# Kernel tuning notes

Measured on AMD Instinct MI355X. Metric: run time of the kernel, lower is better.

Reference implementation:

```python
import jax, jax.numpy as jnp
import numpy as np

SAMPLE_RATE = 256
WIN = 64          # round(256*250/1000)
HOP = 32          # round(256*125/1000)
HIDDEN = 512
PER_CHAN = 8
MAX_CH = 64
_EEG_BANDS = ((0.5, 4.0), (4.0, 8.0), (8.0, 13.0), (13.0, 30.0), (30.0, 100.0))

_FREQS = np.fft.rfftfreq(WIN, d=1.0 / SAMPLE_RATE)
_BAND_MASKS = [np.logical_and(_FREQS >= lo, _FREQS < hi) for (lo, hi) in _EEG_BANDS]


def _sinusoidal_1d(n, dim, dtype=jnp.float32):
    pos = jnp.arange(n, dtype=jnp.float32)[:, None]
    half = dim // 2
    div = jnp.exp(jnp.arange(half, dtype=jnp.float32) * (-np.log(10000.0) / half))
    ang = pos * div[None, :]
    pe = jnp.zeros((n, dim), dtype=jnp.float32)
    pe = pe.at[:, 0::2].set(jnp.sin(ang))
    pe = pe.at[:, 1::2].set(jnp.cos(ang))
    return pe.astype(dtype)


def setup_inputs() -> dict:
    key = jax.random.key(0)
    k = jax.random.split(key, 5)
    B, T, C = 8, 65536, 64
    return {
        "signal": jax.random.normal(k[0], (B, T, C), dtype=jnp.float32),
        "chan_w": 0.02 * jax.random.normal(k[1], (MAX_CH, 7, PER_CHAN), dtype=jnp.float32),
        "chan_b": 0.02 * jax.random.normal(k[2], (MAX_CH, PER_CHAN), dtype=jnp.float32),
        "mix_w": 0.02 * jax.random.normal(k[3], (HIDDEN, MAX_CH * PER_CHAN), dtype=jnp.float32),
        "marker": 0.02 * jax.random.normal(k[4], (HIDDEN,), dtype=jnp.float32),
    }


def reference(signal, chan_w, chan_b, mix_w, marker):
    B, T, C = signal.shape  # C == MAX_CH, no padding/mask branch
    Tw = (T - WIN) // HOP + 1
    idx = jnp.arange(Tw)[:, None] * HOP + jnp.arange(WIN)[None, :]
    x = jnp.transpose(signal[:, idx, :], (0, 1, 3, 2))
    # spectral features
    mag = jnp.abs(jnp.fft.rfft(x, axis=-1))
    band_feats = jnp.stack(
        [mag[..., m].mean(axis=-1) if m.any() else jnp.zeros(mag.shape[:-1], mag.dtype)
         for m in _BAND_MASKS],
        axis=-1,
    )  # (B, Tw, C, 5)
    mean = x.mean(axis=-1, keepdims=True)
    std = jnp.std(x, axis=-1, ddof=1, keepdims=True)  # torch std is unbiased
    feats = jnp.concatenate([band_feats, mean, std], axis=-1)  # (B, Tw, C, 7)
    # per-channel projection + bias
    emb = jnp.einsum("btcf,cfp->btcp", feats, chan_w) + chan_b[None, None]
    flat = emb.reshape(B, Tw, MAX_CH * PER_CHAN)
    z = flat @ mix_w.T  # (B, Tw, HIDDEN)
    z = z + _sinusoidal_1d(Tw, HIDDEN, z.dtype)[None]
    mk = jnp.broadcast_to(marker[None, None, :], (B, 1, HIDDEN))
    return jnp.concatenate([mk, z], axis=1)  # (B, 1+Tw, HIDDEN)
```

## Files before the change

kernel.cpp:

```cpp
#include <hip/hip_runtime.h>
#include <stdint.h>

#define TW_N 2047
#define BATCH 8
#define T_LEN 65536
#define NCH 64
#define HID 512
#define NWIN (BATCH * TW_N)

typedef unsigned short ushortT;

__device__ __forceinline__ ushortT f2b(float f) {
  union { float f; uint32_t i; } v; v.f = f;
  uint32_t r = v.i + 0x7fffu + ((v.i >> 16) & 1u);
  return (ushortT)(r >> 16);
}
__device__ __forceinline__ uint32_t pk2(float lo, float hi) {
  return (uint32_t)f2b(lo) | ((uint32_t)f2b(hi) << 16);
}

__device__ __forceinline__ void gload_lds16(const void* g, void* l) {
  __builtin_amdgcn_global_load_lds(
      (const __attribute__((address_space(1))) uint32_t*)g,
      (__attribute__((address_space(3))) uint32_t*)l, 16, 0, 0);
}

constexpr float CQ[17] = {
  1.0f, 0.9951847267f, 0.9807852804f, 0.9569403357f, 0.9238795325f,
  0.8819212643f, 0.8314696123f, 0.7730104534f, 0.7071067812f, 0.6343932842f,
  0.5555702330f, 0.4713967368f, 0.3826834324f, 0.2902846773f, 0.1950903220f,
  0.0980171403f, 0.0f };
constexpr float cos64(int m) {
  m &= 63;
  return (m <= 16) ? CQ[m] : (m < 32) ? -CQ[32 - m] : (m < 48) ? -CQ[m - 32] : CQ[64 - m];
}
constexpr float sin64(int m) { return cos64(m - 16); }
struct TwTab { float c[24][32]; float s[24][32]; };
constexpr TwTab make_tab() {
  TwTab t{};
  for (int i = 0; i < 24; ++i)
    for (int j = 0; j < 32; ++j) {
      int m = ((i + 1) * j) & 63;
      t.c[i][j] = cos64(m);
      t.s[i][j] = sin64(m);
    }
  return t;
}
constexpr TwTab TT = make_tab();

__device__ ushortT Bpack[HID * HID];

__global__ __launch_bounds__(256) void prep_kernel(
    const float* __restrict__ marker, const float* __restrict__ Bw,
    float* __restrict__ out)
{
  const int gid = blockIdx.x * 256 + threadIdx.x;
  if (blockIdx.x < 16) {
    out[(size_t)(gid >> 9) * (2048 * 512) + (gid & 511)] = marker[gid & 511];
  } else {
    const int i = (gid - 4096) * 8;
    const float4 f0 = *(const float4*)(Bw + i);
    const float4 f1 = *(const float4*)(Bw + i + 4);
    uint4 u;
    u.x = pk2(f0.x, f0.y); u.y = pk2(f0.z, f0.w);
    u.z = pk2(f1.x, f1.y); u.w = pk2(f1.z, f1.w);
    *(uint4*)(Bpack + i) = u;
  }
}

__global__ __launch_bounds__(256) void feat_embed_kernel(
    const float* __restrict__ sig, const float* __restrict__ chw,
    const float* __restrict__ chb, ushortT* __restrict__ flatB)
{
  const int tid = threadIdx.x;
  const int c = tid & 63;
  const int gw = blockIdx.x * 4 + (tid >> 6);
  const int b = gw >> 8;
  const int run = gw & 255;
  const int tw0 = run * 8;
  const int nw = (tw0 + 8 <= TW_N) ? 8 : (TW_N - tw0);
  const float* sg = sig + ((size_t)b * T_LEN + (size_t)tw0 * 32) * NCH + c;
  const float* wr = chw + c * 56;

  float A[32], Bh[32], O[32], R[32];
#pragma unroll
  for (int t = 0; t < 32; ++t) A[t] = sg[t * 64];
#pragma unroll
  for (int t = 0; t < 32; ++t) Bh[t] = sg[(t + 32) * 64];

#pragma unroll 1
  for (int l = 0; l < nw; ++l) {
    {
      int hrow = (tw0 + l + 2) * 32;
      hrow = hrow < (T_LEN - 32) ? hrow : (T_LEN - 32);
      const float* pn = sig + ((size_t)b * T_LEN + hrow) * NCH + c;
#pragma unroll
      for (int t = 0; t < 32; ++t) R[t] = pn[t * 64];
    }

    float sum = 0.f, sumsq = 0.f;
#pragma unroll
    for (int t = 0; t < 32; ++t) {
      O[t] = A[t] - Bh[t];
      A[t] = A[t] + Bh[t];
      sum += A[t];
      sumsq = fmaf(A[t], A[t], fmaf(O[t], O[t], sumsq));
    }

    float b1 = 0.f, b2 = 0.f, b3 = 0.f, b4 = 0.f;
#pragma unroll
    for (int i = 0; i < 24; ++i) {
      const int k = i + 1;
      float re = 0.f, im = 0.f;
#pragma unroll
      for (int t = 0; t < 32; ++t) {
        const float v = (k & 1) ? O[t] : A[t];
        re = fmaf(v, TT.c[i][t], re);
        im = fmaf(v, TT.s[i][t], im);
      }
      const float mag = __builtin_amdgcn_sqrtf(fmaf(re, re, im * im));
      if (k == 1) b1 += mag;
      else if (k < 4) b2 += mag;
      else if (k < 8) b3 += mag;
      else b4 += mag;
    }

    const float mean = sum * (1.f / 64.f);
    const float var = (sumsq * 0.5f - sum * sum * (1.f / 64.f)) * (1.f / 63.f);
    const float sd = __builtin_amdgcn_sqrtf(fmaxf(var, 0.f));

    const float f1 = b1, f2 = b2 * 0.5f, f3 = b3 * 0.25f, f4 = b4 * (1.f / 17.f);
    float emb[8];
#pragma unroll
    for (int p = 0; p < 8; ++p) emb[p] = chb[c * 8 + p];
#pragma unroll
    for (int p = 0; p < 8; ++p) {
      float e = emb[p];
      e = fmaf(f1, wr[8 + p], e);
      e = fmaf(f2, wr[16 + p], e);
      e = fmaf(f3, wr[24 + p], e);
      e = fmaf(f4, wr[32 + p], e);
      e = fmaf(mean, wr[40 + p], e);
      e = fmaf(sd, wr[48 + p], e);
      emb[p] = e;
    }

    uint32_t pka[4];
#pragma unroll
    for (int q = 0; q < 4; ++q) pka[q] = pk2(emb[2 * q], emb[2 * q + 1]);
    const int w = b * TW_N + tw0 + l;
    *(uint4*)(flatB + (size_t)w * HID + c * 8) = make_uint4(pka[0], pka[1], pka[2], pka[3]);

#pragma unroll
    for (int t = 0; t < 32; ++t) { A[t] = Bh[t]; Bh[t] = R[t]; }
  }
}

typedef __attribute__((ext_vector_type(8))) short short8;
typedef __attribute__((ext_vector_type(4))) float f32x4;

__global__ __launch_bounds__(256) void mix_gemm_kernel(
    const ushortT* __restrict__ A,
    float* __restrict__ out)
{
  __shared__ ushortT As[3][128 * 32];
  __shared__ ushortT Bs[3][128 * 32];

  const int tid = threadIdx.x;
  const int lane = tid & 63;
  const int wv = tid >> 6;
  const int wm = wv >> 1, wn = wv & 1;
  const int fr = lane & 15;
  const int fq = lane >> 4;

  const int n0 = blockIdx.x * 128;
  const int m0 = blockIdx.y * 128;

  const int srow = tid >> 2;
  const int sko = (tid & 3) * 8;

  f32x4 acc[4][4];
#pragma unroll
  for (int i = 0; i < 4; ++i)
#pragma unroll
    for (int j = 0; j < 4; ++j) acc[i][j] = (f32x4){0.f, 0.f, 0.f, 0.f};

  int am0 = m0 + srow;       am0 = am0 < NWIN ? am0 : NWIN - 1;
  int am1 = m0 + 64 + srow;  am1 = am1 < NWIN ? am1 : NWIN - 1;
  const ushortT* ga0 = A + (size_t)am0 * HID + sko;
  const ushortT* ga1 = A + (size_t)am1 * HID + sko;
  const ushortT* gb0 = Bpack + (size_t)(n0 + srow) * HID + sko;
  const ushortT* gb1 = Bpack + (size_t)(n0 + 64 + srow) * HID + sko;

#define STAGE(buf, kt) do {                                                    \
    const int ko_ = (kt) * 32;                                                 \
    gload_lds16(ga0 + ko_, (char*)&As[buf][0] + tid * 16);                     \
    gload_lds16(ga1 + ko_, (char*)&As[buf][0] + 4096 + tid * 16);              \
    gload_lds16(gb0 + ko_, (char*)&Bs[buf][0] + tid * 16);                     \
    gload_lds16(gb1 + ko_, (char*)&Bs[buf][0] + 4096 + tid * 16);              \
  } while (0)

  STAGE(0, 0);
  STAGE(1, 1);

  int c0 = 0, c1 = 1, c2 = 2;
  for (int kt = 0; kt < 16; ++kt) {
    if (kt < 14) {
      STAGE(c2, kt + 2);
      asm volatile("s_waitcnt vmcnt(8)\n\ts_barrier" ::: "memory");
    } else if (kt == 14) {
      asm volatile("s_waitcnt vmcnt(4)\n\ts_barrier" ::: "memory");
    } else {
      asm volatile("s_waitcnt vmcnt(0)\n\ts_barrier" ::: "memory");
    }

    short8 af[4], bf[4];
#pragma unroll
    for (int mt = 0; mt < 4; ++mt)
      af[mt] = *(const short8*)&As[c0][(wm * 64 + mt * 16 + fr) * 32 + fq * 8];
#pragma unroll
    for (int nt = 0; nt < 4; ++nt)
      bf[nt] = *(const short8*)&Bs[c0][(wn * 64 + nt * 16 + fr) * 32 + fq * 8];
#pragma unroll
    for (int mt = 0; mt < 4; ++mt)
#pragma unroll
      for (int nt = 0; nt < 4; ++nt)
        acc[mt][nt] = __builtin_amdgcn_mfma_f32_16x16x32_bf16(af[mt], bf[nt], acc[mt][nt], 0, 0, 0);

    asm volatile("s_barrier" ::: "memory");
    const int tmp = c0; c0 = c1; c1 = c2; c2 = tmp;
  }
#undef STAGE

#pragma unroll
  for (int nt = 0; nt < 4; ++nt) {
    const int ng = n0 + wn * 64 + nt * 16 + fr;
    const float dv = __expf(-0.03597789208f * (float)(ng >> 1));
    const bool odd = (ng & 1);
#pragma unroll
    for (int mt = 0; mt < 4; ++mt) {
#pragma unroll
      for (int r = 0; r < 4; ++r) {
        const int mg = m0 + wm * 64 + mt * 16 + fq * 4 + r;
        if (mg < NWIN) {
          const int bb = mg / TW_N;
          const int tw = mg - bb * TW_N;
          const float ang = (float)tw * dv;
          const float pev = odd ? __cosf(ang) : __sinf(ang);
          out[((size_t)(bb * 2048 + 1 + tw)) * HID + ng] = acc[mt][nt][r] + pev;
        }
      }
    }
  }
}

extern "C" void kernel_launch(void* const* d_in, const int* in_sizes, int n_in,
                              void* d_out, int out_size, void* d_ws, size_t ws_size,
                              hipStream_t stream)
{
  const float* sig = (const float*)d_in[0];
  const float* chw = (const float*)d_in[1];
  const float* chb = (const float*)d_in[2];
  const float* mxw = (const float*)d_in[3];
  const float* mkr = (const float*)d_in[4];
  float* out = (float*)d_out;

  ushortT* flatB = (ushortT*)d_ws;

  hipLaunchKernelGGL(prep_kernel, dim3(144), dim3(256), 0, stream, mkr, mxw, out);
  hipLaunchKernelGGL(feat_embed_kernel, dim3(512), dim3(256), 0, stream, sig, chw, chb, flatB);
  hipLaunchKernelGGL(mix_gemm_kernel, dim3(4, 128), dim3(256), 0, stream, flatB, out);
}
```

Measured before the change: 249.8 us.

## Add second radix-2 split to windowed DFT and double feature kernel parallelism

```diff
diff --git a/kernel.cpp b/kernel.cpp
--- a/kernel.cpp
+++ b/kernel.cpp
@@ -35,18 +35,22 @@
   return (m <= 16) ? CQ[m] : (m < 32) ? -CQ[32 - m] : (m < 48) ? -CQ[m - 32] : CQ[64 - m];
 }
 constexpr float sin64(int m) { return cos64(m - 16); }
-struct TwTab { float c[24][32]; float s[24][32]; };
-constexpr TwTab make_tab() {
-  TwTab t{};
-  for (int i = 0; i < 24; ++i)
-    for (int j = 0; j < 32; ++j) {
-      int m = ((i + 1) * j) & 63;
-      t.c[i][j] = cos64(m);
-      t.s[i][j] = sin64(m);
+struct Tw2 { float oc[12][32]; float os[12][32]; float ec[12][16]; float es[12][16]; };
+constexpr Tw2 make2() {
+  Tw2 t{};
+  for (int i = 0; i < 12; ++i)
+    for (int tt = 0; tt < 32; ++tt) {
+      t.oc[i][tt] = cos64((2 * i + 1) * tt);
+      t.os[i][tt] = sin64((2 * i + 1) * tt);
+    }
+  for (int j = 1; j <= 12; ++j)
+    for (int tt = 0; tt < 16; ++tt) {
+      t.ec[j - 1][tt] = cos64(2 * j * tt);
+      t.es[j - 1][tt] = sin64(2 * j * tt);
     }
   return t;
 }
-constexpr TwTab TT = make_tab();
+constexpr Tw2 TW = make2();
 
 __device__ ushortT Bpack[HID * HID];
 
@@ -68,91 +72,106 @@
   }
 }
 
-__global__ __launch_bounds__(256) void feat_embed_kernel(
+#define WIN_BODY(X, Y, l, pf_ofs) do {                                        \
+    float sum = 0.f, so2 = 0.f, se2 = 0.f;                                    \
+    _Pragma("unroll")                                                         \
+    for (int t = 0; t < 32; ++t) {                                            \
+      O[t] = X[t] - Y[t];                                                     \
+      X[t] = X[t] + Y[t];                                                     \
+      so2 = fmaf(O[t], O[t], so2);                                            \
+    }                                                                         \
+    _Pragma("unroll")                                                         \
+    for (int t = 0; t < 16; ++t) {                   \
+      const float u = X[t] + X[t + 16], v = X[t] - X[t + 16];                 \
+      X[t] = u; X[t + 16] = v;                                                \
+      sum += u;                                                               \
+      se2 = fmaf(u, u, fmaf(v, v, se2));                                      \
+    }                                                                         \
+    float b1 = 0.f, b2 = 0.f, b3 = 0.f, b4 = 0.f;                             \
+    _Pragma("unroll")                                                         \
+    for (int j = 1; j <= 12; ++j) {                          \
+      float re = 0.f, im = 0.f;                                               \
+      _Pragma("unroll")                                                       \
+      for (int t = 0; t < 16; ++t) {                                          \
+        const float v = X[(j & 1) * 16 + t];                 \
+        re = fmaf(v, TW.ec[j - 1][t], re);                                    \
+        im = fmaf(v, TW.es[j - 1][t], im);                                    \
+      }                                                                       \
+      const float mag = __builtin_amdgcn_sqrtf(fmaf(re, re, im * im));        \
+      const int k = 2 * j;                                                    \
+      if (k < 4) b2 += mag; else if (k < 8) b3 += mag; else b4 += mag;        \
+    }                                                                         \
+    if ((pf_ofs) >= 0) {                        \
+      const float* pn = sg + (size_t)(pf_ofs) * (32 * NCH);                   \
+      _Pragma("unroll")                                                       \
+      for (int t = 0; t < 32; ++t) X[t] = pn[t * 64];                         \
+    }                                                                         \
+    _Pragma("unroll")                                                         \
+    for (int i = 0; i < 12; ++i) {                  \
+      float re = 0.f, im = 0.f;                                               \
+      _Pragma("unroll")                                                       \
+      for (int t = 0; t < 32; ++t) {                                          \
+        re = fmaf(O[t], TW.oc[i][t], re);                                     \
+        im = fmaf(O[t], TW.os[i][t], im);                                     \
+      }                                                                       \
+      const float mag = __builtin_amdgcn_sqrtf(fmaf(re, re, im * im));        \
+      const int k = 2 * i + 1;                                                \
+      if (k == 1) b1 += mag;                                                  \
+      else if (k < 4) b2 += mag;                                              \
+      else if (k < 8) b3 += mag;                                              \
+      else b4 += mag;                                                         \
+    }                                                                         \
+    const float mean = sum * (1.f / 64.f);                                    \
+    const float var =                                                         \
+        (se2 * 0.25f + so2 * 0.5f - sum * sum * (1.f / 64.f)) * (1.f / 63.f); \
+    const float sd = __builtin_amdgcn_sqrtf(fmaxf(var, 0.f));                 \
+    const float f1 = b1, f2 = b2 * 0.5f, f3 = b3 * 0.25f,                     \
+                f4 = b4 * (1.f / 17.f);                                       \
+    float emb[8];                                                             \
+    _Pragma("unroll")                                                         \
+    for (int p = 0; p < 8; ++p) {                                             \
+      float e = cbp[p];                                                       \
+      e = fmaf(f1, wr[8 + p], e);                                             \
+      e = fmaf(f2, wr[16 + p], e);                                            \
+      e = fmaf(f3, wr[24 + p], e);                                            \
+      e = fmaf(f4, wr[32 + p], e);                                            \
+      e = fmaf(mean, wr[40 + p], e);                                          \
+      e = fmaf(sd, wr[48 + p], e);                                            \
+      emb[p] = e;                                                             \
+    }                                                                         \
+    uint32_t pka[4];                                                          \
+    _Pragma("unroll")                                                         \
+    for (int q = 0; q < 4; ++q) pka[q] = pk2(emb[2 * q], emb[2 * q + 1]);     \
+    *(uint4*)(flatB + (size_t)(wbase + (l)) * HID + c * 8) =                  \
+        make_uint4(pka[0], pka[1], pka[2], pka[3]);                           \
+  } while (0)
+
+__global__ __launch_bounds__(256, 4) void feat_embed_kernel(
     const float* __restrict__ sig, const float* __restrict__ chw,
     const float* __restrict__ chb, ushortT* __restrict__ flatB)
 {
   const int tid = threadIdx.x;
   const int c = tid & 63;
   const int gw = blockIdx.x * 4 + (tid >> 6);
-  const int b = gw >> 8;
-  const int run = gw & 255;
-  const int tw0 = run * 8;
-  const int nw = (tw0 + 8 <= TW_N) ? 8 : (TW_N - tw0);
+  const int b = gw >> 9;
+  const int r = gw & 511;
+  int tw0 = r * 4;
+  if (tw0 > TW_N - 4) tw0 = TW_N - 4;
+  const int wbase = b * TW_N + tw0;
   const float* sg = sig + ((size_t)b * T_LEN + (size_t)tw0 * 32) * NCH + c;
   const float* wr = chw + c * 56;
-
-  float A[32], Bh[32], O[32], R[32];
+  const float* cbp = chb + c * 8;
+
+  float A[32], Bh[32], O[32];
 #pragma unroll
   for (int t = 0; t < 32; ++t) A[t] = sg[t * 64];
 #pragma unroll
   for (int t = 0; t < 32; ++t) Bh[t] = sg[(t + 32) * 64];
 
 #pragma unroll 1
-  for (int l = 0; l < nw; ++l) {
-    {
-      int hrow = (tw0 + l + 2) * 32;
-      hrow = hrow < (T_LEN - 32) ? hrow : (T_LEN - 32);
-      const float* pn = sig + ((size_t)b * T_LEN + hrow) * NCH + c;
-#pragma unroll
-      for (int t = 0; t < 32; ++t) R[t] = pn[t * 64];
-    }
-
-    float sum = 0.f, sumsq = 0.f;
-#pragma unroll
-    for (int t = 0; t < 32; ++t) {
-      O[t] = A[t] - Bh[t];
-      A[t] = A[t] + Bh[t];
-      sum += A[t];
-      sumsq = fmaf(A[t], A[t], fmaf(O[t], O[t], sumsq));
-    }
-
-    float b1 = 0.f, b2 = 0.f, b3 = 0.f, b4 = 0.f;
-#pragma unroll
-    for (int i = 0; i < 24; ++i) {
-      const int k = i + 1;
-      float re = 0.f, im = 0.f;
-#pragma unroll
-      for (int t = 0; t < 32; ++t) {
-        const float v = (k & 1) ? O[t] : A[t];
-        re = fmaf(v, TT.c[i][t], re);
-        im = fmaf(v, TT.s[i][t], im);
-      }
-      const float mag = __builtin_amdgcn_sqrtf(fmaf(re, re, im * im));
-      if (k == 1) b1 += mag;
-      else if (k < 4) b2 += mag;
-      else if (k < 8) b3 += mag;
-      else b4 += mag;
-    }
-
-    const float mean = sum * (1.f / 64.f);
-    const float var = (sumsq * 0.5f - sum * sum * (1.f / 64.f)) * (1.f / 63.f);
-    const float sd = __builtin_amdgcn_sqrtf(fmaxf(var, 0.f));
-
-    const float f1 = b1, f2 = b2 * 0.5f, f3 = b3 * 0.25f, f4 = b4 * (1.f / 17.f);
-    float emb[8];
-#pragma unroll
-    for (int p = 0; p < 8; ++p) emb[p] = chb[c * 8 + p];
-#pragma unroll
-    for (int p = 0; p < 8; ++p) {
-      float e = emb[p];
-      e = fmaf(f1, wr[8 + p], e);
-      e = fmaf(f2, wr[16 + p], e);
-      e = fmaf(f3, wr[24 + p], e);
-      e = fmaf(f4, wr[32 + p], e);
-      e = fmaf(mean, wr[40 + p], e);
-      e = fmaf(sd, wr[48 + p], e);
-      emb[p] = e;
-    }
-
-    uint32_t pka[4];
-#pragma unroll
-    for (int q = 0; q < 4; ++q) pka[q] = pk2(emb[2 * q], emb[2 * q + 1]);
-    const int w = b * TW_N + tw0 + l;
-    *(uint4*)(flatB + (size_t)w * HID + c * 8) = make_uint4(pka[0], pka[1], pka[2], pka[3]);
-
-#pragma unroll
-    for (int t = 0; t < 32; ++t) { A[t] = Bh[t]; Bh[t] = R[t]; }
+  for (int l = 0; l < 4; l += 2) {
+    WIN_BODY(A, Bh, l, l + 2);
+    WIN_BODY(Bh, A, l + 1, (l == 0) ? 3 : -1);
   }
 }
 
@@ -268,6 +287,6 @@
   ushortT* flatB = (ushortT*)d_ws;
 
   hipLaunchKernelGGL(prep_kernel, dim3(144), dim3(256), 0, stream, mkr, mxw, out);
-  hipLaunchKernelGGL(feat_embed_kernel, dim3(512), dim3(256), 0, stream, sig, chw, chb, flatB);
+  hipLaunchKernelGGL(feat_embed_kernel, dim3(1024), dim3(256), 0, stream, sig, chw, chb, flatB);
   hipLaunchKernelGGL(mix_gemm_kernel, dim3(4, 128), dim3(256), 0, stream, flatB, out);
 }
```

Result: slower. 356.1 us (+42.6%).

## Split DFT into even/odd radix-2 stages and map one window per wave

Applied to the files above, without the earlier changes.

```diff
diff --git a/kernel.cpp b/kernel.cpp
--- a/kernel.cpp
+++ b/kernel.cpp
@@ -35,18 +35,22 @@
   return (m <= 16) ? CQ[m] : (m < 32) ? -CQ[32 - m] : (m < 48) ? -CQ[m - 32] : CQ[64 - m];
 }
 constexpr float sin64(int m) { return cos64(m - 16); }
-struct TwTab { float c[24][32]; float s[24][32]; };
-constexpr TwTab make_tab() {
-  TwTab t{};
-  for (int i = 0; i < 24; ++i)
-    for (int j = 0; j < 32; ++j) {
-      int m = ((i + 1) * j) & 63;
-      t.c[i][j] = cos64(m);
-      t.s[i][j] = sin64(m);
+struct Tw2 { float oc[12][32]; float os[12][32]; float ec[12][16]; float es[12][16]; };
+constexpr Tw2 make2() {
+  Tw2 t{};
+  for (int i = 0; i < 12; ++i)
+    for (int tt = 0; tt < 32; ++tt) {
+      t.oc[i][tt] = cos64((2 * i + 1) * tt);
+      t.os[i][tt] = sin64((2 * i + 1) * tt);
+    }
+  for (int j = 1; j <= 12; ++j)
+    for (int tt = 0; tt < 16; ++tt) {
+      t.ec[j - 1][tt] = cos64(2 * j * tt);
+      t.es[j - 1][tt] = sin64(2 * j * tt);
     }
   return t;
 }
-constexpr TwTab TT = make_tab();
+constexpr Tw2 TW = make2();
 
 __device__ ushortT Bpack[HID * HID];
 
@@ -68,92 +72,108 @@
   }
 }
 
-__global__ __launch_bounds__(256) void feat_embed_kernel(
+__global__ __launch_bounds__(256) __attribute__((amdgpu_waves_per_eu(4)))
+void feat_embed_kernel(
     const float* __restrict__ sig, const float* __restrict__ chw,
     const float* __restrict__ chb, ushortT* __restrict__ flatB)
 {
   const int tid = threadIdx.x;
   const int c = tid & 63;
-  const int gw = blockIdx.x * 4 + (tid >> 6);
-  const int b = gw >> 8;
-  const int run = gw & 255;
-  const int tw0 = run * 8;
-  const int nw = (tw0 + 8 <= TW_N) ? 8 : (TW_N - tw0);
-  const float* sg = sig + ((size_t)b * T_LEN + (size_t)tw0 * 32) * NCH + c;
+  const int w = blockIdx.x * 4 + (tid >> 6);
+  const int b = w / TW_N;
+  const int tw = w - b * TW_N;
+  const float* sg = sig + ((size_t)b * T_LEN + (size_t)tw * 32) * NCH + c;
   const float* wr = chw + c * 56;
-
-  float A[32], Bh[32], O[32], R[32];
-#pragma unroll
-  for (int t = 0; t < 32; ++t) A[t] = sg[t * 64];
-#pragma unroll
-  for (int t = 0; t < 32; ++t) Bh[t] = sg[(t + 32) * 64];
-
-#pragma unroll 1
-  for (int l = 0; l < nw; ++l) {
-    {
-      int hrow = (tw0 + l + 2) * 32;
-      hrow = hrow < (T_LEN - 32) ? hrow : (T_LEN - 32);
-      const float* pn = sig + ((size_t)b * T_LEN + hrow) * NCH + c;
-#pragma unroll
-      for (int t = 0; t < 32; ++t) R[t] = pn[t * 64];
-    }
-
-    float sum = 0.f, sumsq = 0.f;
-#pragma unroll
-    for (int t = 0; t < 32; ++t) {
-      O[t] = A[t] - Bh[t];
-      A[t] = A[t] + Bh[t];
-      sum += A[t];
-      sumsq = fmaf(A[t], A[t], fmaf(O[t], O[t], sumsq));
-    }
-
-    float b1 = 0.f, b2 = 0.f, b3 = 0.f, b4 = 0.f;
-#pragma unroll
-    for (int i = 0; i < 24; ++i) {
-      const int k = i + 1;
-      float re = 0.f, im = 0.f;
-#pragma unroll
-      for (int t = 0; t < 32; ++t) {
-        const float v = (k & 1) ? O[t] : A[t];
-        re = fmaf(v, TT.c[i][t], re);
-        im = fmaf(v, TT.s[i][t], im);
-      }
-      const float mag = __builtin_amdgcn_sqrtf(fmaf(re, re, im * im));
-      if (k == 1) b1 += mag;
-      else if (k < 4) b2 += mag;
-      else if (k < 8) b3 += mag;
-      else b4 += mag;
-    }
-
-    const float mean = sum * (1.f / 64.f);
-    const float var = (sumsq * 0.5f - sum * sum * (1.f / 64.f)) * (1.f / 63.f);
-    const float sd = __builtin_amdgcn_sqrtf(fmaxf(var, 0.f));
-
-    const float f1 = b1, f2 = b2 * 0.5f, f3 = b3 * 0.25f, f4 = b4 * (1.f / 17.f);
-    float emb[8];
-#pragma unroll
-    for (int p = 0; p < 8; ++p) emb[p] = chb[c * 8 + p];
-#pragma unroll
-    for (int p = 0; p < 8; ++p) {
-      float e = emb[p];
-      e = fmaf(f1, wr[8 + p], e);
-      e = fmaf(f2, wr[16 + p], e);
-      e = fmaf(f3, wr[24 + p], e);
-      e = fmaf(f4, wr[32 + p], e);
-      e = fmaf(mean, wr[40 + p], e);
-      e = fmaf(sd, wr[48 + p], e);
-      emb[p] = e;
-    }
-
-    uint32_t pka[4];
-#pragma unroll
-    for (int q = 0; q < 4; ++q) pka[q] = pk2(emb[2 * q], emb[2 * q + 1]);
-    const int w = b * TW_N + tw0 + l;
-    *(uint4*)(flatB + (size_t)w * HID + c * 8) = make_uint4(pka[0], pka[1], pka[2], pka[3]);
-
-#pragma unroll
-    for (int t = 0; t < 32; ++t) { A[t] = Bh[t]; Bh[t] = R[t]; }
-  }
+  const float* cbp = chb + c * 8;
+
+  float X[32], Y[32];
+#pragma unroll
+  for (int t = 0; t < 32; ++t) X[t] = sg[t * 64];
+#pragma unroll
+  for (int t = 0; t < 32; ++t) Y[t] = sg[(t + 32) * 64];
+
+  float sum = 0.f, so2 = 0.f, se2 = 0.f;
+#pragma unroll
+  for (int t = 0; t < 32; ++t) {
+    const float e = X[t] + Y[t];
+    const float o = X[t] - Y[t];
+    X[t] = e; Y[t] = o;
+    so2 = fmaf(o, o, so2);
+  }
+#pragma unroll
+  for (int t = 0; t < 16; ++t) {
+    const float u = X[t] + X[t + 16], v = X[t] - X[t + 16];
+    X[t] = u; X[t + 16] = v;
+    sum += u;
+    se2 = fmaf(u, u, fmaf(v, v, se2));
+  }
+
+  float ro[12], io[12];
+#pragma unroll
+  for (int i = 0; i < 12; ++i) { ro[i] = 0.f; io[i] = 0.f; }
+#pragma unroll
+  for (int t = 0; t < 32; ++t) {
+    const float o = Y[t];
+#pragma unroll
+    for (int i = 0; i < 12; ++i) {
+      ro[i] = fmaf(o, TW.oc[i][t], ro[i]);
+      io[i] = fmaf(o, TW.os[i][t], io[i]);
+    }
+  }
+  float b1 = 0.f, b2 = 0.f, b3 = 0.f, b4 = 0.f;
+#pragma unroll
+  for (int i = 0; i < 12; ++i) {
+    const float mag = __builtin_amdgcn_sqrtf(fmaf(ro[i], ro[i], io[i] * io[i]));
+    const int k = 2 * i + 1;
+    if (k == 1) b1 += mag;
+    else if (k < 4) b2 += mag;
+    else if (k < 8) b3 += mag;
+    else b4 += mag;
+  }
+
+  float re_[12], ie_[12];
+#pragma unroll
+  for (int j = 0; j < 12; ++j) { re_[j] = 0.f; ie_[j] = 0.f; }
+#pragma unroll
+  for (int t = 0; t < 16; ++t) {
+#pragma unroll
+    for (int j = 1; j <= 12; ++j) {
+      const float vv = X[(j & 1) * 16 + t];
+      re_[j - 1] = fmaf(vv, TW.ec[j - 1][t], re_[j - 1]);
+      ie_[j - 1] = fmaf(vv, TW.es[j - 1][t], ie_[j - 1]);
+    }
+  }
+#pragma unroll
+  for (int j = 1; j <= 12; ++j) {
+    const float mag = __builtin_amdgcn_sqrtf(
+        fmaf(re_[j - 1], re_[j - 1], ie_[j - 1] * ie_[j - 1]));
+    const int k = 2 * j;
+    if (k < 4) b2 += mag; else if (k < 8) b3 += mag; else b4 += mag;
+  }
+
+  const float mean = sum * (1.f / 64.f);
+  const float var =
+      (se2 * 0.25f + so2 * 0.5f - sum * sum * (1.f / 64.f)) * (1.f / 63.f);
+  const float sd = __builtin_amdgcn_sqrtf(fmaxf(var, 0.f));
+
+  const float f1 = b1, f2 = b2 * 0.5f, f3 = b3 * 0.25f, f4 = b4 * (1.f / 17.f);
+  float emb[8];
+#pragma unroll
+  for (int p = 0; p < 8; ++p) {
+    float e = cbp[p];
+    e = fmaf(f1, wr[8 + p], e);
+    e = fmaf(f2, wr[16 + p], e);
+    e = fmaf(f3, wr[24 + p], e);
+    e = fmaf(f4, wr[32 + p], e);
+    e = fmaf(mean, wr[40 + p], e);
+    e = fmaf(sd, wr[48 + p], e);
+    emb[p] = e;
+  }
+
+  uint32_t pka[4];
+#pragma unroll
+  for (int q = 0; q < 4; ++q) pka[q] = pk2(emb[2 * q], emb[2 * q + 1]);
+  *(uint4*)(flatB + (size_t)w * HID + c * 8) = make_uint4(pka[0], pka[1], pka[2], pka[3]);
 }
 
 typedef __attribute__((ext_vector_type(8))) short short8;
@@ -268,6 +288,6 @@
   ushortT* flatB = (ushortT*)d_ws;
 
   hipLaunchKernelGGL(prep_kernel, dim3(144), dim3(256), 0, stream, mkr, mxw, out);
-  hipLaunchKernelGGL(feat_embed_kernel, dim3(512), dim3(256), 0, stream, sig, chw, chb, flatB);
+  hipLaunchKernelGGL(feat_embed_kernel, dim3(4094), dim3(256), 0, stream, sig, chw, chb, flatB);
   hipLaunchKernelGGL(mix_gemm_kernel, dim3(4, 128), dim3(256), 0, stream, flatB, out);
 }
```

Measured after the change: 240.3 us. -3.8%, faster.
